# Kernel tuning notes

Measured on AMD Instinct MI355X. Metric: run time of the kernel, lower is better.

The kernel has to match this reference:

```python
import jax, jax.numpy as jnp
import numpy as np

EPS_STAB = 1e-12
SINKHORN_EPS = 0.05
SINKHORN_ITERS = 20
TAU = 0.3


def l2norm(x):
    # F.normalize(x, dim=1, p=2) with eps clamp
    n = jnp.linalg.norm(x, axis=1, keepdims=True)
    return x / jnp.maximum(n, 1e-12)


def sinkhorn(out):
    # out: [B, K] scores; returns soft assignments [B, K]
    Q = jnp.exp(out / SINKHORN_EPS).T          # [K, B]
    K, B = Q.shape                              # static ints
    Q = Q / jnp.sum(Q)

    def body(Q, _):
        u = jnp.sum(Q, axis=1, keepdims=True)   # row sums [K,1]
        has_zero = jnp.any(u == 0)
        Q = jnp.where(has_zero, Q + EPS_STAB, Q)
        u = jnp.where(has_zero, jnp.sum(Q, axis=1, keepdims=True), u)
        Q = Q / u / K
        Q = Q / jnp.sum(Q, axis=0, keepdims=True) / B
        return Q, None

    Q, _ = jax.lax.scan(body, Q, None, length=SINKHORN_ITERS)
    return (Q * B).T                            # [B, K]


def setup_inputs() -> dict:
    key = jax.random.key(0)
    k1, k2, k3 = jax.random.split(key, 3)
    N, D, K = 32768, 512, 512
    z1 = jax.random.normal(k1, (N, D), dtype=jnp.float32)
    z2 = jax.random.normal(k2, (N, D), dtype=jnp.float32)
    # xavier-uniform-ish init for prototype weight [K, D]
    limit = float(np.sqrt(6.0 / (K + D)))
    weight = jax.random.uniform(k3, (K, D), dtype=jnp.float32, minval=-limit, maxval=limit)
    return {"z1": z1, "z2": z2, "weight": weight}


def reference(z1, z2, weight):
    # weight is normalized in-place under no_grad in torch: straight-through
    wn = weight + jax.lax.stop_gradient(l2norm(weight) - weight)  # [K, D]
    zc1 = l2norm(z1) @ wn.T                     # [N, K]
    zc2 = l2norm(z2) @ wn.T                     # [N, K]
    q1 = sinkhorn(jax.lax.stop_gradient(zc1))
    q2 = sinkhorn(jax.lax.stop_gradient(zc2))
    l1 = -jnp.mean(jnp.sum(q1 * jax.nn.log_softmax(zc2 / TAU, axis=1), axis=1))
    l2 = -jnp.mean(jnp.sum(q2 * jax.nn.log_softmax(zc1 / TAU, axis=1), axis=1))
    return l1 + l2
```

## Files before the change

### kernel.cpp

```cpp
#include <hip/hip_runtime.h>
#include <stdint.h>

#define NROWS 32768
#define DDIM  512
#define KDIM  512

__device__ __forceinline__ float b2f(unsigned short u) {
  return __uint_as_float(((unsigned int)u) << 16);
}
__device__ __forceinline__ unsigned short f2bf(float f) {
  unsigned int u = __float_as_uint(f);
  u += 0x7FFFu + ((u >> 16) & 1u);
  return (unsigned short)(u >> 16);
}

typedef __attribute__((ext_vector_type(8))) short bf16x8;
typedef __attribute__((ext_vector_type(4))) float f32x4;

__global__ __launch_bounds__(256) void prep_kernel(
    const float* __restrict__ z1, const float* __restrict__ z2,
    const float* __restrict__ w, float* __restrict__ rnorm,
    unsigned short* __restrict__ wnb) {
  const int tid = threadIdx.x;
  const int wv = tid >> 6, ln = tid & 63;
  const int row = blockIdx.x * 4 + wv;
  const float* src;
  if (row < NROWS)        src = z1 + (size_t)row * DDIM;
  else if (row < 2*NROWS) src = z2 + (size_t)(row - NROWS) * DDIM;
  else                    src = w  + (size_t)(row - 2*NROWS) * DDIM;
  float4 v0 = ((const float4*)src)[ln*2];
  float4 v1 = ((const float4*)src)[ln*2+1];
  float ss = v0.x*v0.x + v0.y*v0.y + v0.z*v0.z + v0.w*v0.w
           + v1.x*v1.x + v1.y*v1.y + v1.z*v1.z + v1.w*v1.w;
  #pragma unroll
  for (int off = 1; off < 64; off <<= 1) ss += __shfl_xor(ss, off);
  float rn = 1.0f / fmaxf(sqrtf(ss), 1e-12f);
  if (row < 2*NROWS) {
    if (ln == 0) rnorm[row] = rn;
  } else {
    int r = row - 2*NROWS;
    ushort4 o0 = make_ushort4(f2bf(v0.x*rn), f2bf(v0.y*rn), f2bf(v0.z*rn), f2bf(v0.w*rn));
    ushort4 o1 = make_ushort4(f2bf(v1.x*rn), f2bf(v1.y*rn), f2bf(v1.z*rn), f2bf(v1.w*rn));
    ushort4* dst = (ushort4*)(wnb + (size_t)r*DDIM + ln*8);
    dst[0] = o0; dst[1] = o1;
  }
}

__global__ void initvecs_kernel(float* __restrict__ T, float* __restrict__ out) {
  int i = blockIdx.x * 256 + threadIdx.x;
  if (i < 20 * 1024) T[i] = 0.f;
  if (i == 0) out[0] = 0.f;
}

__global__ __launch_bounds__(256) void gemm_kernel(
    const float* __restrict__ z1, const float* __restrict__ z2,
    const float* __restrict__ rnorm, const unsigned short* __restrict__ wnb,
    unsigned short* __restrict__ zc) {
  constexpr int LDT = 40;
  __shared__ unsigned short As[128 * LDT];
  __shared__ unsigned short Bs[128 * LDT];
  const int tid = threadIdx.x;
  const int colBase = blockIdx.x * 128;
  const int rowBase = blockIdx.y * 128;
  const float* Aptr = (rowBase < NROWS) ? (z1 + (size_t)rowBase * DDIM)
                                        : (z2 + (size_t)(rowBase - NROWS) * DDIM);
  const int wv = tid >> 6, ln = tid & 63;
  const int wm = wv & 1, wn = wv >> 1;
  const int lrow = ln & 15, quad = ln >> 4;

  f32x4 acc[4][4] = {};

  for (int k0 = 0; k0 < DDIM; k0 += 32) {
    #pragma unroll
    for (int i = 0; i < 4; i++) {
      int idx = i * 256 + tid;
      int r = idx >> 3;
      int kk = (idx & 7) * 4;
      float4 v = *(const float4*)(Aptr + (size_t)r * DDIM + k0 + kk);
      float rn = rnorm[rowBase + r];
      ushort4 o = make_ushort4(f2bf(v.x*rn), f2bf(v.y*rn), f2bf(v.z*rn), f2bf(v.w*rn));
      *(ushort4*)(&As[r * LDT + kk]) = o;
    }
    #pragma unroll
    for (int i = 0; i < 2; i++) {
      int idx = i * 256 + tid;
      int r = idx >> 2;
      int kk = (idx & 3) * 8;
      float4 v = *(const float4*)(wnb + (size_t)(colBase + r) * DDIM + k0 + kk);
      *(float4*)(&Bs[r * LDT + kk]) = v;
    }
    __syncthreads();
    bf16x8 af[4], bfr[4];
    #pragma unroll
    for (int mi = 0; mi < 4; mi++)
      af[mi] = *(const bf16x8*)(&As[(64*wm + 16*mi + lrow) * LDT + quad*8]);
    #pragma unroll
    for (int ni = 0; ni < 4; ni++)
      bfr[ni] = *(const bf16x8*)(&Bs[(64*wn + 16*ni + lrow) * LDT + quad*8]);
    #pragma unroll
    for (int mi = 0; mi < 4; mi++)
      #pragma unroll
      for (int ni = 0; ni < 4; ni++)
        acc[mi][ni] = __builtin_amdgcn_mfma_f32_16x16x32_bf16(
            af[mi], bfr[ni], acc[mi][ni], 0, 0, 0);
    __syncthreads();
  }
  #pragma unroll
  for (int mi = 0; mi < 4; mi++)
    #pragma unroll
    for (int ni = 0; ni < 4; ni++)
      #pragma unroll
      for (int r = 0; r < 4; r++) {
        size_t grow = (size_t)rowBase + 64*wm + 16*mi + quad*4 + r;
        int gcol = colBase + 64*wn + 16*ni + lrow;
        zc[grow * KDIM + gcol] = f2bf(acc[mi][ni][r]);
      }
}

__global__ __launch_bounds__(1024) void pass_kernel(
    const unsigned short* __restrict__ zc,
    const float* __restrict__ Tprev, float* __restrict__ Tnext, int mode) {
  __shared__ float red[16 * 512];
  const int tid = threadIdx.x;
  const int wv = tid >> 6, ln = tid & 63;
  const int gw = blockIdx.x * 16 + wv;
  const size_t row0 = (size_t)gw * 8;
  const int mat = blockIdx.x >> 8;
  float a[8];
  if (mode) {
    #pragma unroll
    for (int j = 0; j < 8; j++) a[j] = 1.0f / (512.0f * Tprev[mat*512 + ln*8 + j]);
  }
  float acc[8] = {0,0,0,0,0,0,0,0};
  const unsigned short* base = zc + row0 * 512 + ln * 8;
  #pragma unroll
  for (int r = 0; r < 8; r++) {
    const ushort4* p = (const ushort4*)(base + (size_t)r * 512);
    ushort4 u0 = p[0], u1 = p[1];
    float e[8];
    e[0]=__expf(b2f(u0.x)*20.f); e[1]=__expf(b2f(u0.y)*20.f);
    e[2]=__expf(b2f(u0.z)*20.f); e[3]=__expf(b2f(u0.w)*20.f);
    e[4]=__expf(b2f(u1.x)*20.f); e[5]=__expf(b2f(u1.y)*20.f);
    e[6]=__expf(b2f(u1.z)*20.f); e[7]=__expf(b2f(u1.w)*20.f);
    if (mode) {
      float part = e[0]*a[0]+e[1]*a[1]+e[2]*a[2]+e[3]*a[3]
                 + e[4]*a[4]+e[5]*a[5]+e[6]*a[6]+e[7]*a[7];
      #pragma unroll
      for (int off = 1; off < 64; off <<= 1) part += __shfl_xor(part, off);
      float b = 1.0f / (32768.0f * part);
      #pragma unroll
      for (int j = 0; j < 8; j++) acc[j] += e[j] * b;
    } else {
      #pragma unroll
      for (int j = 0; j < 8; j++) acc[j] += e[j];
    }
  }
  #pragma unroll
  for (int j = 0; j < 8; j++) red[wv*512 + ln*8 + j] = acc[j];
  __syncthreads();
  if (tid < 512) {
    float s = 0.f;
    #pragma unroll
    for (int w = 0; w < 16; w++) s += red[w*512 + tid];
    unsafeAtomicAdd(&Tnext[mat*512 + tid], s);
  }
}

__global__ __launch_bounds__(1024) void loss_kernel(
    const unsigned short* __restrict__ zc,
    const float* __restrict__ T19, float* __restrict__ out) {
  const int tid = threadIdx.x;
  const int wv = tid >> 6, ln = tid & 63;
  const int gw = blockIdx.x * 16 + wv;
  const size_t row0 = (size_t)gw * 4;
  float a1[8], a2[8];
  #pragma unroll
  for (int j = 0; j < 8; j++) {
    a1[j] = 1.0f / (512.0f * T19[ln*8 + j]);
    a2[j] = 1.0f / (512.0f * T19[512 + ln*8 + j]);
  }
  const float invTau = 1.0f / 0.3f;
  float part = 0.f;
  for (int r = 0; r < 4; r++) {
    size_t b = row0 + r;
    const ushort4* p1 = (const ushort4*)(zc + b * 512 + ln * 8);
    const ushort4* p2 = (const ushort4*)(zc + (b + NROWS) * 512 + ln * 8);
    ushort4 u10 = p1[0], u11 = p1[1], u20 = p2[0], u21 = p2[1];
    float zf1[8], zf2[8];
    zf1[0]=b2f(u10.x); zf1[1]=b2f(u10.y); zf1[2]=b2f(u10.z); zf1[3]=b2f(u10.w);
    zf1[4]=b2f(u11.x); zf1[5]=b2f(u11.y); zf1[6]=b2f(u11.z); zf1[7]=b2f(u11.w);
    zf2[0]=b2f(u20.x); zf2[1]=b2f(u20.y); zf2[2]=b2f(u20.z); zf2[3]=b2f(u20.w);
    zf2[4]=b2f(u21.x); zf2[5]=b2f(u21.y); zf2[6]=b2f(u21.z); zf2[7]=b2f(u21.w);
    float m1 = -1e30f, m2 = -1e30f;
    #pragma unroll
    for (int j = 0; j < 8; j++) { m1 = fmaxf(m1, zf1[j]); m2 = fmaxf(m2, zf2[j]); }
    #pragma unroll
    for (int off = 1; off < 64; off <<= 1) {
      m1 = fmaxf(m1, __shfl_xor(m1, off));
      m2 = fmaxf(m2, __shfl_xor(m2, off));
    }
    float se1 = 0.f, se2 = 0.f;
    #pragma unroll
    for (int j = 0; j < 8; j++) {
      se1 += __expf((zf1[j] - m1) * invTau);
      se2 += __expf((zf2[j] - m2) * invTau);
    }
    #pragma unroll
    for (int off = 1; off < 64; off <<= 1) {
      se1 += __shfl_xor(se1, off);
      se2 += __shfl_xor(se2, off);
    }
    float ls1 = m1 * invTau + __logf(se1);
    float ls2 = m2 * invTau + __logf(se2);
    float s1 = 0.f, n1 = 0.f, s2 = 0.f, n2 = 0.f;
    #pragma unroll
    for (int j = 0; j < 8; j++) {
      float e1 = __expf(zf1[j] * 20.f) * a1[j];
      s1 += e1; n1 += e1 * (zf2[j] * invTau - ls2);
      float e2 = __expf(zf2[j] * 20.f) * a2[j];
      s2 += e2; n2 += e2 * (zf1[j] * invTau - ls1);
    }
    #pragma unroll
    for (int off = 1; off < 64; off <<= 1) {
      s1 += __shfl_xor(s1, off); n1 += __shfl_xor(n1, off);
      s2 += __shfl_xor(s2, off); n2 += __shfl_xor(n2, off);
    }
    part += n1 / s1 + n2 / s2;
  }
  __shared__ float red[16];
  if (ln == 0) red[wv] = part;
  __syncthreads();
  if (tid == 0) {
    float s = 0.f;
    #pragma unroll
    for (int w = 0; w < 16; w++) s += red[w];
    unsafeAtomicAdd(out, -s * (1.0f / 32768.0f));
  }
}

extern "C" void kernel_launch(void* const* d_in, const int* in_sizes, int n_in,
                              void* d_out, int out_size, void* d_ws, size_t ws_size,
                              hipStream_t stream) {
  (void)in_sizes; (void)n_in; (void)out_size; (void)ws_size;
  const float* z1 = (const float*)d_in[0];
  const float* z2 = (const float*)d_in[1];
  const float* w  = (const float*)d_in[2];
  float* out = (float*)d_out;
  char* ws = (char*)d_ws;
  unsigned short* zc    = (unsigned short*)ws;
  float*          rnorm = (float*)(ws + (size_t)67108864);
  unsigned short* wnb   = (unsigned short*)(ws + (size_t)67371008);
  float*          T     = (float*)(ws + (size_t)67895296);

  hipLaunchKernelGGL(prep_kernel, dim3(16512), dim3(256), 0, stream, z1, z2, w, rnorm, wnb);
  hipLaunchKernelGGL(initvecs_kernel, dim3(80), dim3(256), 0, stream, T, out);
  hipLaunchKernelGGL(gemm_kernel, dim3(4, 512), dim3(256), 0, stream, z1, z2, rnorm, wnb, zc);
  hipLaunchKernelGGL(pass_kernel, dim3(512), dim3(1024), 0, stream, zc, T, T, 0);
  for (int i = 1; i < 20; i++)
    hipLaunchKernelGGL(pass_kernel, dim3(512), dim3(1024), 0, stream,
                       zc, T + (size_t)(i-1)*1024, T + (size_t)i*1024, 1);
  hipLaunchKernelGGL(loss_kernel, dim3(512), dim3(1024), 0, stream, zc, T + 19*1024, out);
}
```

Measured before the change: 691.2 us.

## Fuse Sinkhorn passes and loss into one persistent cooperative kernel with register-resident scores

Replaces the 20 separate Sinkhorn pass launches and the loss launch with a single cooperative kernel of 256 blocks. Each wave keeps its 16 rows of both score matrices in registers as bf16, and iterations are separated by grid.sync(). This avoids re-reading the 64 MB score matrix from memory on every iteration and removes per-launch overhead. In exchange it uses many registers, needs all blocks resident at once, and adds a grid-wide barrier per iteration. The exponentials are still recomputed every pass.

```diff
diff --git a/kernel.cpp b/kernel.cpp
--- a/kernel.cpp
+++ b/kernel.cpp
@@ -1,5 +1,8 @@
 #include <hip/hip_runtime.h>
+#include <hip/hip_cooperative_groups.h>
 #include <stdint.h>
+
+namespace cg = cooperative_groups;
 
 #define NROWS 32768
 #define DDIM  512
@@ -12,6 +15,9 @@
   unsigned int u = __float_as_uint(f);
   u += 0x7FFFu + ((u >> 16) & 1u);
   return (unsigned short)(u >> 16);
+}
+__device__ __forceinline__ float dev_load(const float* p) {
+  return __hip_atomic_load(p, __ATOMIC_RELAXED, __HIP_MEMORY_SCOPE_AGENT);
 }
 
 typedef __attribute__((ext_vector_type(8))) short bf16x8;
@@ -117,124 +123,144 @@
       }
 }
 
-__global__ __launch_bounds__(1024) void pass_kernel(
+__global__ __launch_bounds__(512, 2) void sink_kernel(
     const unsigned short* __restrict__ zc,
-    const float* __restrict__ Tprev, float* __restrict__ Tnext, int mode) {
-  __shared__ float red[16 * 512];
+    float* __restrict__ T, float* __restrict__ out) {
+  cg::grid_group grid = cg::this_grid();
+  __shared__ float red[8 * 1024];
   const int tid = threadIdx.x;
   const int wv = tid >> 6, ln = tid & 63;
-  const int gw = blockIdx.x * 16 + wv;
-  const size_t row0 = (size_t)gw * 8;
-  const int mat = blockIdx.x >> 8;
-  float a[8];
-  if (mode) {
-    #pragma unroll
-    for (int j = 0; j < 8; j++) a[j] = 1.0f / (512.0f * Tprev[mat*512 + ln*8 + j]);
-  }
-  float acc[8] = {0,0,0,0,0,0,0,0};
-  const unsigned short* base = zc + row0 * 512 + ln * 8;
+  const int col0 = ln * 8;
+  const size_t row0 = (size_t)blockIdx.x * 128 + (size_t)wv * 16;
+
+  bf16x8 d1[16], d2[16];
   #pragma unroll
-  for (int r = 0; r < 8; r++) {
-    const ushort4* p = (const ushort4*)(base + (size_t)r * 512);
-    ushort4 u0 = p[0], u1 = p[1];
-    float e[8];
-    e[0]=__expf(b2f(u0.x)*20.f); e[1]=__expf(b2f(u0.y)*20.f);
-    e[2]=__expf(b2f(u0.z)*20.f); e[3]=__expf(b2f(u0.w)*20.f);
-    e[4]=__expf(b2f(u1.x)*20.f); e[5]=__expf(b2f(u1.y)*20.f);
-    e[6]=__expf(b2f(u1.z)*20.f); e[7]=__expf(b2f(u1.w)*20.f);
-    if (mode) {
-      float part = e[0]*a[0]+e[1]*a[1]+e[2]*a[2]+e[3]*a[3]
-                 + e[4]*a[4]+e[5]*a[5]+e[6]*a[6]+e[7]*a[7];
-      #pragma unroll
-      for (int off = 1; off < 64; off <<= 1) part += __shfl_xor(part, off);
-      float b = 1.0f / (32768.0f * part);
-      #pragma unroll
-      for (int j = 0; j < 8; j++) acc[j] += e[j] * b;
-    } else {
-      #pragma unroll
-      for (int j = 0; j < 8; j++) acc[j] += e[j];
-    }
-  }
-  #pragma unroll
-  for (int j = 0; j < 8; j++) red[wv*512 + ln*8 + j] = acc[j];
-  __syncthreads();
-  if (tid < 512) {
-    float s = 0.f;
-    #pragma unroll
-    for (int w = 0; w < 16; w++) s += red[w*512 + tid];
-    unsafeAtomicAdd(&Tnext[mat*512 + tid], s);
-  }
-}
-
-__global__ __launch_bounds__(1024) void loss_kernel(
-    const unsigned short* __restrict__ zc,
-    const float* __restrict__ T19, float* __restrict__ out) {
-  const int tid = threadIdx.x;
-  const int wv = tid >> 6, ln = tid & 63;
-  const int gw = blockIdx.x * 16 + wv;
-  const size_t row0 = (size_t)gw * 4;
-  float a1[8], a2[8];
-  #pragma unroll
-  for (int j = 0; j < 8; j++) {
-    a1[j] = 1.0f / (512.0f * T19[ln*8 + j]);
-    a2[j] = 1.0f / (512.0f * T19[512 + ln*8 + j]);
-  }
-  const float invTau = 1.0f / 0.3f;
-  float part = 0.f;
-  for (int r = 0; r < 4; r++) {
-    size_t b = row0 + r;
-    const ushort4* p1 = (const ushort4*)(zc + b * 512 + ln * 8);
-    const ushort4* p2 = (const ushort4*)(zc + (b + NROWS) * 512 + ln * 8);
-    ushort4 u10 = p1[0], u11 = p1[1], u20 = p2[0], u21 = p2[1];
-    float zf1[8], zf2[8];
-    zf1[0]=b2f(u10.x); zf1[1]=b2f(u10.y); zf1[2]=b2f(u10.z); zf1[3]=b2f(u10.w);
-    zf1[4]=b2f(u11.x); zf1[5]=b2f(u11.y); zf1[6]=b2f(u11.z); zf1[7]=b2f(u11.w);
-    zf2[0]=b2f(u20.x); zf2[1]=b2f(u20.y); zf2[2]=b2f(u20.z); zf2[3]=b2f(u20.w);
-    zf2[4]=b2f(u21.x); zf2[5]=b2f(u21.y); zf2[6]=b2f(u21.z); zf2[7]=b2f(u21.w);
-    float m1 = -1e30f, m2 = -1e30f;
-    #pragma unroll
-    for (int j = 0; j < 8; j++) { m1 = fmaxf(m1, zf1[j]); m2 = fmaxf(m2, zf2[j]); }
-    #pragma unroll
-    for (int off = 1; off < 64; off <<= 1) {
-      m1 = fmaxf(m1, __shfl_xor(m1, off));
-      m2 = fmaxf(m2, __shfl_xor(m2, off));
-    }
-    float se1 = 0.f, se2 = 0.f;
+  for (int r = 0; r < 16; r++) {
+    d1[r] = *(const bf16x8*)(zc + (row0 + r) * KDIM + col0);
+    d2[r] = *(const bf16x8*)(zc + (row0 + r + (size_t)NROWS) * KDIM + col0);
+  }
+
+  #pragma unroll 1
+  for (int it = 0; it < 20; it++) {
+    float a1[8], a2[8];
+    if (it > 0) {
+      const float* Tp = T + (size_t)(it - 1) * 1024;
+      #pragma unroll
+      for (int j = 0; j < 8; j++) {
+        a1[j] = 1.0f / (512.0f * dev_load(Tp + col0 + j));
+        a2[j] = 1.0f / (512.0f * dev_load(Tp + 512 + col0 + j));
+      }
+    }
+    float acc1[8] = {0,0,0,0,0,0,0,0};
+    float acc2[8] = {0,0,0,0,0,0,0,0};
+    #pragma unroll
+    for (int r = 0; r < 16; r++) {
+      float e[8];
+      #pragma unroll
+      for (int j = 0; j < 8; j++) e[j] = __expf(b2f((unsigned short)d1[r][j]) * 20.f);
+      if (it > 0) {
+        float part = e[0]*a1[0]+e[1]*a1[1]+e[2]*a1[2]+e[3]*a1[3]
+                   + e[4]*a1[4]+e[5]*a1[5]+e[6]*a1[6]+e[7]*a1[7];
+        #pragma unroll
+        for (int off = 1; off < 64; off <<= 1) part += __shfl_xor(part, off);
+        float bb = 1.0f / (32768.0f * part);
+        #pragma unroll
+        for (int j = 0; j < 8; j++) acc1[j] += e[j] * bb;
+      } else {
+        #pragma unroll
+        for (int j = 0; j < 8; j++) acc1[j] += e[j];
+      }
+      #pragma unroll
+      for (int j = 0; j < 8; j++) e[j] = __expf(b2f((unsigned short)d2[r][j]) * 20.f);
+      if (it > 0) {
+        float part = e[0]*a2[0]+e[1]*a2[1]+e[2]*a2[2]+e[3]*a2[3]
+                   + e[4]*a2[4]+e[5]*a2[5]+e[6]*a2[6]+e[7]*a2[7];
+        #pragma unroll
+        for (int off = 1; off < 64; off <<= 1) part += __shfl_xor(part, off);
+        float bb = 1.0f / (32768.0f * part);
+        #pragma unroll
+        for (int j = 0; j < 8; j++) acc2[j] += e[j] * bb;
+      } else {
+        #pragma unroll
+        for (int j = 0; j < 8; j++) acc2[j] += e[j];
+      }
+    }
+    #pragma unroll
+    for (int j = 0; j < 8; j++) red[wv*1024 + col0 + j] = acc1[j];
+    #pragma unroll
+    for (int j = 0; j < 8; j++) red[wv*1024 + 512 + col0 + j] = acc2[j];
+    __syncthreads();
+    float s0 = 0.f, s1 = 0.f;
+    #pragma unroll
+    for (int w = 0; w < 8; w++) { s0 += red[w*1024 + tid]; s1 += red[w*1024 + 512 + tid]; }
+    float* Tn = T + (size_t)it * 1024;
+    unsafeAtomicAdd(&Tn[tid], s0);
+    unsafeAtomicAdd(&Tn[512 + tid], s1);
+    grid.sync();
+  }
+
+  {
+    const float* Tl = T + (size_t)19 * 1024;
+    float a1[8], a2[8];
     #pragma unroll
     for (int j = 0; j < 8; j++) {
-      se1 += __expf((zf1[j] - m1) * invTau);
-      se2 += __expf((zf2[j] - m2) * invTau);
-    }
-    #pragma unroll
-    for (int off = 1; off < 64; off <<= 1) {
-      se1 += __shfl_xor(se1, off);
-      se2 += __shfl_xor(se2, off);
-    }
-    float ls1 = m1 * invTau + __logf(se1);
-    float ls2 = m2 * invTau + __logf(se2);
-    float s1 = 0.f, n1 = 0.f, s2 = 0.f, n2 = 0.f;
-    #pragma unroll
-    for (int j = 0; j < 8; j++) {
-      float e1 = __expf(zf1[j] * 20.f) * a1[j];
-      s1 += e1; n1 += e1 * (zf2[j] * invTau - ls2);
-      float e2 = __expf(zf2[j] * 20.f) * a2[j];
-      s2 += e2; n2 += e2 * (zf1[j] * invTau - ls1);
-    }
-    #pragma unroll
-    for (int off = 1; off < 64; off <<= 1) {
-      s1 += __shfl_xor(s1, off); n1 += __shfl_xor(n1, off);
-      s2 += __shfl_xor(s2, off); n2 += __shfl_xor(n2, off);
-    }
-    part += n1 / s1 + n2 / s2;
-  }
-  __shared__ float red[16];
-  if (ln == 0) red[wv] = part;
-  __syncthreads();
-  if (tid == 0) {
-    float s = 0.f;
-    #pragma unroll
-    for (int w = 0; w < 16; w++) s += red[w];
-    unsafeAtomicAdd(out, -s * (1.0f / 32768.0f));
+      a1[j] = 1.0f / (512.0f * dev_load(Tl + col0 + j));
+      a2[j] = 1.0f / (512.0f * dev_load(Tl + 512 + col0 + j));
+    }
+    const float invTau = 1.0f / 0.3f;
+    float part = 0.f;
+    #pragma unroll
+    for (int r = 0; r < 16; r++) {
+      float zf1[8], zf2[8];
+      #pragma unroll
+      for (int j = 0; j < 8; j++) {
+        zf1[j] = b2f((unsigned short)d1[r][j]);
+        zf2[j] = b2f((unsigned short)d2[r][j]);
+      }
+      float m1 = -1e30f, m2 = -1e30f;
+      #pragma unroll
+      for (int j = 0; j < 8; j++) { m1 = fmaxf(m1, zf1[j]); m2 = fmaxf(m2, zf2[j]); }
+      #pragma unroll
+      for (int off = 1; off < 64; off <<= 1) {
+        m1 = fmaxf(m1, __shfl_xor(m1, off));
+        m2 = fmaxf(m2, __shfl_xor(m2, off));
+      }
+      float se1 = 0.f, se2 = 0.f;
+      #pragma unroll
+      for (int j = 0; j < 8; j++) {
+        se1 += __expf((zf1[j] - m1) * invTau);
+        se2 += __expf((zf2[j] - m2) * invTau);
+      }
+      #pragma unroll
+      for (int off = 1; off < 64; off <<= 1) {
+        se1 += __shfl_xor(se1, off);
+        se2 += __shfl_xor(se2, off);
+      }
+      float ls1 = m1 * invTau + __logf(se1);
+      float ls2 = m2 * invTau + __logf(se2);
+      float s1 = 0.f, n1 = 0.f, s2 = 0.f, n2 = 0.f;
+      #pragma unroll
+      for (int j = 0; j < 8; j++) {
+        float e1 = __expf(zf1[j] * 20.f) * a1[j];
+        s1 += e1; n1 += e1 * (zf2[j] * invTau - ls2);
+        float e2 = __expf(zf2[j] * 20.f) * a2[j];
+        s2 += e2; n2 += e2 * (zf1[j] * invTau - ls1);
+      }
+      #pragma unroll
+      for (int off = 1; off < 64; off <<= 1) {
+        s1 += __shfl_xor(s1, off); n1 += __shfl_xor(n1, off);
+        s2 += __shfl_xor(s2, off); n2 += __shfl_xor(n2, off);
+      }
+      part += n1 / s1 + n2 / s2;
+    }
+    if (ln == 0) red[wv] = part;
+    __syncthreads();
+    if (tid == 0) {
+      float s = 0.f;
+      #pragma unroll
+      for (int w = 0; w < 8; w++) s += red[w];
+      unsafeAtomicAdd(out, -s * (1.0f / 32768.0f));
+    }
   }
 }
 
@@ -255,9 +281,9 @@
   hipLaunchKernelGGL(prep_kernel, dim3(16512), dim3(256), 0, stream, z1, z2, w, rnorm, wnb);
   hipLaunchKernelGGL(initvecs_kernel, dim3(80), dim3(256), 0, stream, T, out);
   hipLaunchKernelGGL(gemm_kernel, dim3(4, 512), dim3(256), 0, stream, z1, z2, rnorm, wnb, zc);
-  hipLaunchKernelGGL(pass_kernel, dim3(512), dim3(1024), 0, stream, zc, T, T, 0);
-  for (int i = 1; i < 20; i++)
-    hipLaunchKernelGGL(pass_kernel, dim3(512), dim3(1024), 0, stream,
-                       zc, T + (size_t)(i-1)*1024, T + (size_t)i*1024, 1);
-  hipLaunchKernelGGL(loss_kernel, dim3(512), dim3(1024), 0, stream, zc, T + 19*1024, out);
-}
+  {
+    void* args[] = {(void*)&zc, (void*)&T, (void*)&out};
+    hipLaunchCooperativeKernel((const void*)sink_kernel, dim3(256), dim3(512),
+                               args, 0, stream);
+  }
+}
```

Measured after the change: 1.378 ms. 99.4% more time.

## Fuse first Sinkhorn pass into GEMM epilogue and remap blocks per XCD

Applied to the files above, without the earlier changes.

The GEMM epilogue now computes exp(score/eps) column sums from the bf16-rounded outputs and accumulates them into the first Sinkhorn vector with atomics, so the separate mode-0 pass over the full score matrix is dropped. The GEMM launch also becomes a 1D grid, with block IDs remapped so that consecutive row blocks land on the same XCD and share L2 for A tiles. This saves one full read of the 64MB bf16 score matrix plus a launch, at the cost of extra exp work, LDS atomics and global float atomics in the GEMM, and a non-deterministic summation order.

```diff
diff --git a/kernel.cpp b/kernel.cpp
--- a/kernel.cpp
+++ b/kernel.cpp
@@ -55,13 +55,18 @@
 __global__ __launch_bounds__(256) void gemm_kernel(
     const float* __restrict__ z1, const float* __restrict__ z2,
     const float* __restrict__ rnorm, const unsigned short* __restrict__ wnb,
-    unsigned short* __restrict__ zc) {
+    unsigned short* __restrict__ zc, float* __restrict__ T0) {
   constexpr int LDT = 40;
   __shared__ unsigned short As[128 * LDT];
   __shared__ unsigned short Bs[128 * LDT];
-  const int tid = threadIdx.x;
-  const int colBase = blockIdx.x * 128;
-  const int rowBase = blockIdx.y * 128;
+  __shared__ float colsum[128];
+  const int tid = threadIdx.x;
+  const int bid = blockIdx.x;
+  const int xcd = bid & 7, slot = bid >> 3;
+  const int rowBlk = xcd * 64 + (slot >> 2);
+  const int colBlk = slot & 3;
+  const int colBase = colBlk * 128;
+  const int rowBase = rowBlk * 128;
   const float* Aptr = (rowBase < NROWS) ? (z1 + (size_t)rowBase * DDIM)
                                         : (z2 + (size_t)(rowBase - NROWS) * DDIM);
   const int wv = tid >> 6, ln = tid & 63;
@@ -105,16 +110,28 @@
             af[mi], bfr[ni], acc[mi][ni], 0, 0, 0);
     __syncthreads();
   }
-  #pragma unroll
-  for (int mi = 0; mi < 4; mi++)
-    #pragma unroll
-    for (int ni = 0; ni < 4; ni++)
+  if (tid < 128) colsum[tid] = 0.f;
+  __syncthreads();
+  #pragma unroll
+  for (int ni = 0; ni < 4; ni++) {
+    float s = 0.f;
+    #pragma unroll
+    for (int mi = 0; mi < 4; mi++)
       #pragma unroll
       for (int r = 0; r < 4; r++) {
         size_t grow = (size_t)rowBase + 64*wm + 16*mi + quad*4 + r;
         int gcol = colBase + 64*wn + 16*ni + lrow;
-        zc[grow * KDIM + gcol] = f2bf(acc[mi][ni][r]);
+        unsigned short h = f2bf(acc[mi][ni][r]);
+        zc[grow * KDIM + gcol] = h;
+        s += __expf(b2f(h) * 20.f);
       }
+    atomicAdd(&colsum[64*wn + 16*ni + lrow], s);
+  }
+  __syncthreads();
+  if (tid < 128) {
+    int matOff = (rowBase < NROWS) ? 0 : 512;
+    unsafeAtomicAdd(&T0[matOff + colBase + tid], colsum[tid]);
+  }
 }
 
 __global__ __launch_bounds__(1024) void pass_kernel(
@@ -254,8 +271,7 @@
 
   hipLaunchKernelGGL(prep_kernel, dim3(16512), dim3(256), 0, stream, z1, z2, w, rnorm, wnb);
   hipLaunchKernelGGL(initvecs_kernel, dim3(80), dim3(256), 0, stream, T, out);
-  hipLaunchKernelGGL(gemm_kernel, dim3(4, 512), dim3(256), 0, stream, z1, z2, rnorm, wnb, zc);
-  hipLaunchKernelGGL(pass_kernel, dim3(512), dim3(1024), 0, stream, zc, T, T, 0);
+  hipLaunchKernelGGL(gemm_kernel, dim3(2048), dim3(256), 0, stream, z1, z2, rnorm, wnb, zc, T);
   for (int i = 1; i < 20; i++)
     hipLaunchKernelGGL(pass_kernel, dim3(512), dim3(1024), 0, stream,
                        zc, T + (size_t)(i-1)*1024, T + (size_t)i*1024, 1);
```

Measured after the change: 661.7 us. -4.3%, faster.
